# Kernel optimization log

Hardware: AMD Instinct MI355X
Metric: run time of the kernel (lower is better)

The kernel has to match this reference:

```python
import jax, jax.numpy as jnp
import numpy as np

B, T, C = 4, 2048, 1024
H, D = 16, 64  # num_heads, head_dim
WINDOW = 256


def setup_inputs() -> dict:
    key = jax.random.key(0)
    k_x, k_qkv, k_proj, k_qb, k_pb = jax.random.split(key, 5)
    x = jax.random.normal(k_x, (B, T, C), dtype=jnp.float32)
    # xavier-uniform-ish init for qkv weight (as in _reset_parameters)
    lim_qkv = float(np.sqrt(6.0 / (C + 3 * C)))
    qkv_w = jax.random.uniform(k_qkv, (3 * C, C), minval=-lim_qkv, maxval=lim_qkv, dtype=jnp.float32)
    qkv_b = jax.random.normal(k_qb, (3 * C,), dtype=jnp.float32) * 0.02
    lim_p = float(np.sqrt(1.0 / C))
    proj_w = jax.random.uniform(k_proj, (C, C), minval=-lim_p, maxval=lim_p, dtype=jnp.float32)
    proj_b = jax.random.normal(k_pb, (C,), dtype=jnp.float32) * 0.02
    # windowed causal mask: attend to j iff j <= i and i - j < WINDOW
    i = jnp.arange(T)[:, None]
    j = jnp.arange(T)[None, :]
    attn_mask = (j <= i) & (i - j < WINDOW)  # [T, T] bool
    return {"x": x, "attn_mask": attn_mask, "qkv_w": qkv_w, "qkv_b": qkv_b,
            "proj_w": proj_w, "proj_b": proj_b}


def reference(x, attn_mask, qkv_w, qkv_b, proj_w, proj_b):
    qkv = (x @ qkv_w.T + qkv_b).reshape(B, T, 3, H, D)
    qkv = jnp.transpose(qkv, (2, 0, 3, 1, 4))
    q, k, v = qkv[0], qkv[1], qkv[2]
    scale = 1.0 / jnp.sqrt(jnp.asarray(D, dtype=q.dtype))
    scores = jnp.einsum('bhqd,bhkd->bhqk', q, k) * scale  # [B,H,T,T]
    neg = jnp.asarray(jnp.finfo(scores.dtype).min, dtype=scores.dtype)
    scores = jnp.where(attn_mask[None, None], scores, neg)
    attn = jax.nn.softmax(scores, axis=-1)
    out = jnp.einsum('bhqk,bhkd->bhqd', attn, v)  # [B,H,T,D]
    out = jnp.transpose(out, (0, 2, 1, 3)).reshape(B, T, C)
    out = out @ proj_w.T + proj_b
    return out
```

## Files before the change

### kernel.cpp

```cpp
#include <hip/hip_runtime.h>

#define BB 4
#define TT 2048
#define CC 1024
#define HH 16
#define DD 64
#define WIN 256

typedef __attribute__((ext_vector_type(8))) short short8;
typedef __attribute__((ext_vector_type(4))) float floatx4;
typedef unsigned short u16;

typedef __attribute__((address_space(3))) void lds_void;
typedef const __attribute__((address_space(1))) void g_void;

__device__ __forceinline__ void gl_lds16(const u16* g, u16* l) {
    __builtin_amdgcn_global_load_lds((g_void*)g, (lds_void*)l, 16, 0, 0);
}

__device__ __forceinline__ float bf2f(u16 u) {
    union { unsigned int i; float f; } v; v.i = ((unsigned int)u) << 16; return v.f;
}
__device__ __forceinline__ u16 f2bf(float f) {
    union { float f; unsigned int i; } v; v.f = f;
    unsigned int x = v.i;
    x += ((x >> 16) & 1u) + 0x7FFFu;
    return (u16)(x >> 16);
}

__global__ void cvt_all(const float* __restrict__ x, const float* __restrict__ qw,
                        const float* __restrict__ pw,
                        u16* __restrict__ xb, u16* __restrict__ wb, u16* __restrict__ pwb) {
    int bid = blockIdx.x;
    const float* src; u16* dst; int off;
    if (bid < 4096)      { src = x;  dst = xb;  off = bid; }
    else if (bid < 5632) { src = qw; dst = wb;  off = bid - 4096; }
    else                 { src = pw; dst = pwb; off = bid - 5632; }
    int i = (off * 256 + (int)threadIdx.x) * 8;
    float4 a = *(const float4*)(src + i);
    float4 b = *(const float4*)(src + i + 4);
    u16 o[8] = { f2bf(a.x), f2bf(a.y), f2bf(a.z), f2bf(a.w),
                 f2bf(b.x), f2bf(b.y), f2bf(b.z), f2bf(b.w) };
    *(uint4*)(dst + i) = *(const uint4*)o;
}


__global__ __launch_bounds__(256) void gemm_qkv(
    const u16* __restrict__ A, const u16* __restrict__ Bw,
    const float* __restrict__ bias,
    u16* __restrict__ Qb, u16* __restrict__ Kb, u16* __restrict__ Vb)
{
    const int K = CC;
    __shared__ u16 As[4096];
    __shared__ u16 Bs[4096];
    const int tid = threadIdx.x;
    const int wave = tid >> 6, lane = tid & 63;
    const int wm = wave >> 1, wn = wave & 1;
    const int quad = lane >> 4, l15 = lane & 15;
    const int bN = blockIdx.x * 128, bM = blockIdx.y * 128;

    const int srow0 = wave * 16 + (lane >> 2);
    const int srow1 = (wave + 4) * 16 + (lane >> 2);
    const int schunk = ((lane & 3) ^ ((lane >> 3) & 3)) * 8;
    const u16* gA0 = A + (size_t)(bM + srow0) * K + schunk;
    const u16* gA1 = A + (size_t)(bM + srow1) * K + schunk;
    const u16* gB0 = Bw + (size_t)(bN + srow0) * K + schunk;
    const u16* gB1 = Bw + (size_t)(bN + srow1) * K + schunk;
    u16* lA0 = &As[wave * 512];
    u16* lA1 = &As[(wave + 4) * 512];
    u16* lB0 = &Bs[wave * 512];
    u16* lB1 = &Bs[(wave + 4) * 512];

    const int rdoff = l15 * 32 + ((quad ^ ((l15 >> 1) & 3)) * 8);

    floatx4 acc[4][4] = {};

    for (int k0 = 0; k0 < K; k0 += 32) {
        __syncthreads();
        gl_lds16(gA0 + k0, lA0);
        gl_lds16(gA1 + k0, lA1);
        gl_lds16(gB0 + k0, lB0);
        gl_lds16(gB1 + k0, lB1);
        __syncthreads();
        short8 af[4], bf[4];
#pragma unroll
        for (int i = 0; i < 4; ++i) {
            af[i] = *(const short8*)&As[(wm * 4 + i) * 512 + rdoff];
            bf[i] = *(const short8*)&Bs[(wn * 4 + i) * 512 + rdoff];
        }
#pragma unroll
        for (int mi = 0; mi < 4; ++mi)
#pragma unroll
            for (int ni = 0; ni < 4; ++ni)
                acc[mi][ni] = __builtin_amdgcn_mfma_f32_16x16x32_bf16(af[mi], bf[ni], acc[mi][ni], 0, 0, 0);
    }

#pragma unroll
    for (int mi = 0; mi < 4; ++mi)
#pragma unroll
        for (int ni = 0; ni < 4; ++ni) {
            int col = bN + wn * 64 + ni * 16 + l15;
            float bv = bias[col];
            int which = col >> 10, rem = col & 1023;
            int h = rem >> 6, d = rem & 63;
            u16* dst = which == 0 ? Qb : (which == 1 ? Kb : Vb);
#pragma unroll
            for (int rg = 0; rg < 4; ++rg) {
                int row = bM + wm * 64 + mi * 16 + quad * 4 + rg;
                int b = row >> 11, t = row & 2047;
                float v = acc[mi][ni][rg] + bv;
                dst[(((size_t)(b * HH + h)) * TT + t) * DD + d] = f2bf(v);
            }
        }
}

__global__ __launch_bounds__(256) void gemm_proj(
    const u16* __restrict__ A, const u16* __restrict__ Bw,
    const float* __restrict__ bias, float* __restrict__ Out)
{
    const int K = CC;
    __shared__ u16 As[4096];
    __shared__ u16 Bs[4096];
    const int tid = threadIdx.x;
    const int wave = tid >> 6, lane = tid & 63;
    const int wm = wave >> 1, wn = wave & 1;
    const int quad = lane >> 4, l15 = lane & 15;
    const int bN = blockIdx.x * 128, bM = blockIdx.y * 128;

    const int srow0 = wave * 16 + (lane >> 2);
    const int srow1 = (wave + 4) * 16 + (lane >> 2);
    const int schunk = ((lane & 3) ^ ((lane >> 3) & 3)) * 8;
    const u16* gA0 = A + (size_t)(bM + srow0) * K + schunk;
    const u16* gA1 = A + (size_t)(bM + srow1) * K + schunk;
    const u16* gB0 = Bw + (size_t)(bN + srow0) * K + schunk;
    const u16* gB1 = Bw + (size_t)(bN + srow1) * K + schunk;
    u16* lA0 = &As[wave * 512];
    u16* lA1 = &As[(wave + 4) * 512];
    u16* lB0 = &Bs[wave * 512];
    u16* lB1 = &Bs[(wave + 4) * 512];

    const int rdoff = l15 * 32 + ((quad ^ ((l15 >> 1) & 3)) * 8);

    floatx4 acc[4][4] = {};

    for (int k0 = 0; k0 < K; k0 += 32) {
        __syncthreads();
        gl_lds16(gA0 + k0, lA0);
        gl_lds16(gA1 + k0, lA1);
        gl_lds16(gB0 + k0, lB0);
        gl_lds16(gB1 + k0, lB1);
        __syncthreads();
        short8 af[4], bf[4];
#pragma unroll
        for (int i = 0; i < 4; ++i) {
            af[i] = *(const short8*)&As[(wm * 4 + i) * 512 + rdoff];
            bf[i] = *(const short8*)&Bs[(wn * 4 + i) * 512 + rdoff];
        }
#pragma unroll
        for (int mi = 0; mi < 4; ++mi)
#pragma unroll
            for (int ni = 0; ni < 4; ++ni)
                acc[mi][ni] = __builtin_amdgcn_mfma_f32_16x16x32_bf16(af[mi], bf[ni], acc[mi][ni], 0, 0, 0);
    }

#pragma unroll
    for (int mi = 0; mi < 4; ++mi)
#pragma unroll
        for (int ni = 0; ni < 4; ++ni) {
            int col = bN + wn * 64 + ni * 16 + l15;
            float bv = bias[col];
#pragma unroll
            for (int rg = 0; rg < 4; ++rg) {
                int row = bM + wm * 64 + mi * 16 + quad * 4 + rg;
                Out[(size_t)row * CC + col] = acc[mi][ni][rg] + bv;
            }
        }
}

__global__ __launch_bounds__(256) void attn_mfma(
    const u16* __restrict__ Qb, const u16* __restrict__ Kb, const u16* __restrict__ Vb,
    u16* __restrict__ Y)
{
    __shared__ u16 Ks[64][72];
    __shared__ u16 Vt[64][72];
    __shared__ u16 Ps[4][16][72];

    const int tid = threadIdx.x;
    const int wave = tid >> 6, lane = tid & 63;
    const int quad = lane >> 4, l15 = lane & 15;
    const int q0 = blockIdx.x * 64;
    const int bh = blockIdx.y;
    const int b = bh >> 4, h = bh & 15;
    const u16* Qp = Qb + (size_t)bh * TT * DD;
    const u16* Kp = Kb + (size_t)bh * TT * DD;
    const u16* Vp = Vb + (size_t)bh * TT * DD;
    const int qw = q0 + wave * 16;

    short8 qf[2];
    qf[0] = *(const short8*)&Qp[(size_t)(qw + l15) * DD + quad * 8];
    qf[1] = *(const short8*)&Qp[(size_t)(qw + l15) * DD + 32 + quad * 8];

    float m_i[4] = { -1e30f, -1e30f, -1e30f, -1e30f };
    float l_i[4] = { 0.f, 0.f, 0.f, 0.f };
    floatx4 Oacc[4] = {};

    const int kb = (q0 >= WIN) ? (q0 - WIN) : 0;
    for (int j0 = kb; j0 < q0 + 64; j0 += 64) {
        __syncthreads();
#pragma unroll
        for (int it = 0; it < 2; ++it) {
            int slot = tid + it * 256;
            int j = slot >> 3, c8 = (slot & 7) << 3;
            *(uint4*)&Ks[j][c8] = *(const uint4*)&Kp[(size_t)(j0 + j) * DD + c8];
        }
#pragma unroll
        for (int it = 0; it < 2; ++it) {
            int slot = tid + it * 256;
            int j = slot >> 3, d0 = (slot & 7) << 3;
            uint4 raw = *(const uint4*)&Vp[(size_t)(j0 + j) * DD + d0];
            const u16* u = (const u16*)&raw;
#pragma unroll
            for (int i = 0; i < 8; ++i) {
                int d = d0 + i;
                int col = (((j >> 3) ^ (d >> 3)) << 3) + (j & 7);
                Vt[d][col] = u[i];
            }
        }
        __syncthreads();

        floatx4 Sacc[4] = {};
#pragma unroll
        for (int nt = 0; nt < 4; ++nt) {
            short8 kf0 = *(const short8*)&Ks[nt * 16 + l15][quad * 8];
            short8 kf1 = *(const short8*)&Ks[nt * 16 + l15][32 + quad * 8];
            Sacc[nt] = __builtin_amdgcn_mfma_f32_16x16x32_bf16(qf[0], kf0, Sacc[nt], 0, 0, 0);
            Sacc[nt] = __builtin_amdgcn_mfma_f32_16x16x32_bf16(qf[1], kf1, Sacc[nt], 0, 0, 0);
        }

        float mc[4] = { -1e30f, -1e30f, -1e30f, -1e30f };
#pragma unroll
        for (int nt = 0; nt < 4; ++nt)
#pragma unroll
            for (int r = 0; r < 4; ++r) {
                int q = qw + quad * 4 + r;
                int j = j0 + nt * 16 + l15;
                float s = (j <= q && (q - j) < WIN) ? Sacc[nt][r] * 0.125f : -1e30f;
                Sacc[nt][r] = s;
                mc[r] = fmaxf(mc[r], s);
            }
#pragma unroll
        for (int m = 1; m < 16; m <<= 1)
#pragma unroll
            for (int r = 0; r < 4; ++r) mc[r] = fmaxf(mc[r], __shfl_xor(mc[r], m, 64));

        float alpha[4];
#pragma unroll
        for (int r = 0; r < 4; ++r) {
            float mn = fmaxf(m_i[r], mc[r]);
            alpha[r] = __expf(m_i[r] - mn);
            m_i[r] = mn;
        }
        float rs[4] = { 0.f, 0.f, 0.f, 0.f };
#pragma unroll
        for (int nt = 0; nt < 4; ++nt)
#pragma unroll
            for (int r = 0; r < 4; ++r) {
                float s = Sacc[nt][r];
                float p = (s > -1e29f) ? __expf(s - m_i[r]) : 0.f;
                Sacc[nt][r] = p;
                rs[r] += p;
            }
#pragma unroll
        for (int m = 1; m < 16; m <<= 1)
#pragma unroll
            for (int r = 0; r < 4; ++r) rs[r] += __shfl_xor(rs[r], m, 64);
#pragma unroll
        for (int r = 0; r < 4; ++r) l_i[r] = l_i[r] * alpha[r] + rs[r];
#pragma unroll
        for (int dt = 0; dt < 4; ++dt)
#pragma unroll
            for (int r = 0; r < 4; ++r) Oacc[dt][r] *= alpha[r];

#pragma unroll
        for (int nt = 0; nt < 4; ++nt)
#pragma unroll
            for (int r = 0; r < 4; ++r)
                Ps[wave][quad * 4 + r][nt * 16 + l15] = f2bf(Sacc[nt][r]);

#pragma unroll
        for (int ks = 0; ks < 2; ++ks) {
            short8 pf = *(const short8*)&Ps[wave][l15][ks * 32 + quad * 8];
#pragma unroll
            for (int dt = 0; dt < 4; ++dt) {
                int d = dt * 16 + l15;
                int col = (((ks * 4 + quad) ^ (d >> 3)) << 3);
                short8 vf = *(const short8*)&Vt[d][col];
                Oacc[dt] = __builtin_amdgcn_mfma_f32_16x16x32_bf16(pf, vf, Oacc[dt], 0, 0, 0);
            }
        }
    }

    float inv[4];
#pragma unroll
    for (int r = 0; r < 4; ++r) inv[r] = 1.f / l_i[r];
#pragma unroll
    for (int dt = 0; dt < 4; ++dt)
#pragma unroll
        for (int r = 0; r < 4; ++r) {
            int t = qw + quad * 4 + r;
            int d = dt * 16 + l15;
            Y[((size_t)b * TT + t) * CC + h * DD + d] = f2bf(Oacc[dt][r] * inv[r]);
        }
}

extern "C" void kernel_launch(void* const* d_in, const int* in_sizes, int n_in,
                              void* d_out, int out_size, void* d_ws, size_t ws_size,
                              hipStream_t stream) {
    const float* x      = (const float*)d_in[0];
    const float* qkv_w  = (const float*)d_in[2];
    const float* qkv_b  = (const float*)d_in[3];
    const float* proj_w = (const float*)d_in[4];
    const float* proj_b = (const float*)d_in[5];
    float* out = (float*)d_out;

    u16* xb  = (u16*)d_ws;
    u16* wb  = xb  + (size_t)8192 * 1024;
    u16* pwb = wb  + (size_t)3072 * 1024;
    u16* Qb  = pwb + (size_t)1024 * 1024;
    u16* Kb  = Qb  + (size_t)64 * 2048 * 64;
    u16* Vb  = Kb  + (size_t)64 * 2048 * 64;
    u16* Yb  = Vb  + (size_t)64 * 2048 * 64;

    cvt_all<<<6144, 256, 0, stream>>>(x, qkv_w, proj_w, xb, wb, pwb);
    gemm_qkv<<<dim3(24, 64), 256, 0, stream>>>(xb, wb, qkv_b, Qb, Kb, Vb);
    attn_mfma<<<dim3(TT / 64, BB * HH), 256, 0, stream>>>(Qb, Kb, Vb, Yb);
    gemm_proj<<<dim3(8, 64), 256, 0, stream>>>(Yb, pwb, proj_b, out);
}
```

Before: 238.3 us.

## Store V transposed from QKV GEMM and load K/V via direct global-to-LDS

The QKV GEMM epilogue now writes V in a [bh][d][t] transposed layout with packed 4-element stores, so the attention kernel no longer transposes V element by element through LDS. Attention loads K and V tiles with global_load_lds into swizzled LDS buffers and swaps the MFMA operand order so each lane owns one query row. That turns the row max and sum reductions into two shuffles on a single scalar and allows packed P and output stores. The V stores in the GEMM become strided across t, which may cost some write efficiency there.

```diff
diff --git a/kernel.cpp b/kernel.cpp
--- a/kernel.cpp
+++ b/kernel.cpp
@@ -44,11 +44,10 @@
     *(uint4*)(dst + i) = *(const uint4*)o;
 }
 
-
 __global__ __launch_bounds__(256) void gemm_qkv(
     const u16* __restrict__ A, const u16* __restrict__ Bw,
     const float* __restrict__ bias,
-    u16* __restrict__ Qb, u16* __restrict__ Kb, u16* __restrict__ Vb)
+    u16* __restrict__ Qb, u16* __restrict__ Kb, u16* __restrict__ Vtg)
 {
     const int K = CC;
     __shared__ u16 As[4096];
@@ -103,13 +102,18 @@
             float bv = bias[col];
             int which = col >> 10, rem = col & 1023;
             int h = rem >> 6, d = rem & 63;
-            u16* dst = which == 0 ? Qb : (which == 1 ? Kb : Vb);
-#pragma unroll
-            for (int rg = 0; rg < 4; ++rg) {
-                int row = bM + wm * 64 + mi * 16 + quad * 4 + rg;
-                int b = row >> 11, t = row & 2047;
-                float v = acc[mi][ni][rg] + bv;
-                dst[(((size_t)(b * HH + h)) * TT + t) * DD + d] = f2bf(v);
+            int row0 = bM + wm * 64 + mi * 16 + quad * 4;
+            int b = row0 >> 11, t0 = row0 & 2047;
+            if (which == 2) {
+                u16 pk[4];
+#pragma unroll
+                for (int rg = 0; rg < 4; ++rg) pk[rg] = f2bf(acc[mi][ni][rg] + bv);
+                *(uint2*)&Vtg[(((size_t)(b * HH + h)) * DD + d) * TT + t0] = *(const uint2*)pk;
+            } else {
+                u16* dst = which == 0 ? Qb : Kb;
+#pragma unroll
+                for (int rg = 0; rg < 4; ++rg)
+                    dst[(((size_t)(b * HH + h)) * TT + t0 + rg) * DD + d] = f2bf(acc[mi][ni][rg] + bv);
             }
         }
 }
@@ -178,12 +182,12 @@
 }
 
 __global__ __launch_bounds__(256) void attn_mfma(
-    const u16* __restrict__ Qb, const u16* __restrict__ Kb, const u16* __restrict__ Vb,
+    const u16* __restrict__ Qb, const u16* __restrict__ Kb, const u16* __restrict__ Vtg,
     u16* __restrict__ Y)
 {
-    __shared__ u16 Ks[64][72];
-    __shared__ u16 Vt[64][72];
-    __shared__ u16 Ps[4][16][72];
+    __shared__ __align__(16) u16 Ks[4096];
+    __shared__ __align__(16) u16 Vs[4096];
+    __shared__ __align__(16) u16 Ps[4][16][72];
 
     const int tid = threadIdx.x;
     const int wave = tid >> 6, lane = tid & 63;
@@ -193,124 +197,98 @@
     const int b = bh >> 4, h = bh & 15;
     const u16* Qp = Qb + (size_t)bh * TT * DD;
     const u16* Kp = Kb + (size_t)bh * TT * DD;
-    const u16* Vp = Vb + (size_t)bh * TT * DD;
+    const u16* Vp = Vtg + (size_t)bh * DD * TT;
     const int qw = q0 + wave * 16;
+
+    const int lrow = lane >> 3;
+    const int lchunk = ((lane & 7) ^ lrow) << 3;
+    const int s0 = wave * 2, s1 = wave * 2 + 1;
 
     short8 qf[2];
     qf[0] = *(const short8*)&Qp[(size_t)(qw + l15) * DD + quad * 8];
     qf[1] = *(const short8*)&Qp[(size_t)(qw + l15) * DD + 32 + quad * 8];
 
-    float m_i[4] = { -1e30f, -1e30f, -1e30f, -1e30f };
-    float l_i[4] = { 0.f, 0.f, 0.f, 0.f };
+    float m_i = -1e30f, l_i = 0.f;
     floatx4 Oacc[4] = {};
 
+    const int swz = l15 & 7;
     const int kb = (q0 >= WIN) ? (q0 - WIN) : 0;
     for (int j0 = kb; j0 < q0 + 64; j0 += 64) {
         __syncthreads();
-#pragma unroll
-        for (int it = 0; it < 2; ++it) {
-            int slot = tid + it * 256;
-            int j = slot >> 3, c8 = (slot & 7) << 3;
-            *(uint4*)&Ks[j][c8] = *(const uint4*)&Kp[(size_t)(j0 + j) * DD + c8];
-        }
-#pragma unroll
-        for (int it = 0; it < 2; ++it) {
-            int slot = tid + it * 256;
-            int j = slot >> 3, d0 = (slot & 7) << 3;
-            uint4 raw = *(const uint4*)&Vp[(size_t)(j0 + j) * DD + d0];
-            const u16* u = (const u16*)&raw;
-#pragma unroll
-            for (int i = 0; i < 8; ++i) {
-                int d = d0 + i;
-                int col = (((j >> 3) ^ (d >> 3)) << 3) + (j & 7);
-                Vt[d][col] = u[i];
-            }
-        }
+        gl_lds16(&Kp[(size_t)(j0 + s0 * 8 + lrow) * DD + lchunk], &Ks[s0 * 512]);
+        gl_lds16(&Kp[(size_t)(j0 + s1 * 8 + lrow) * DD + lchunk], &Ks[s1 * 512]);
+        gl_lds16(&Vp[(size_t)(s0 * 8 + lrow) * TT + j0 + lchunk], &Vs[s0 * 512]);
+        gl_lds16(&Vp[(size_t)(s1 * 8 + lrow) * TT + j0 + lchunk], &Vs[s1 * 512]);
         __syncthreads();
 
         floatx4 Sacc[4] = {};
 #pragma unroll
-        for (int nt = 0; nt < 4; ++nt) {
-            short8 kf0 = *(const short8*)&Ks[nt * 16 + l15][quad * 8];
-            short8 kf1 = *(const short8*)&Ks[nt * 16 + l15][32 + quad * 8];
-            Sacc[nt] = __builtin_amdgcn_mfma_f32_16x16x32_bf16(qf[0], kf0, Sacc[nt], 0, 0, 0);
-            Sacc[nt] = __builtin_amdgcn_mfma_f32_16x16x32_bf16(qf[1], kf1, Sacc[nt], 0, 0, 0);
-        }
-
-        float mc[4] = { -1e30f, -1e30f, -1e30f, -1e30f };
-#pragma unroll
-        for (int nt = 0; nt < 4; ++nt)
+        for (int ks = 0; ks < 2; ++ks)
+#pragma unroll
+            for (int kt = 0; kt < 4; ++kt) {
+                short8 kf = *(const short8*)&Ks[(kt * 16 + l15) * 64 + (((ks * 4 + quad) ^ swz) << 3)];
+                Sacc[kt] = __builtin_amdgcn_mfma_f32_16x16x32_bf16(kf, qf[ks], Sacc[kt], 0, 0, 0);
+            }
+
+        const int q = qw + l15;
+        float mc = -1e30f;
+#pragma unroll
+        for (int kt = 0; kt < 4; ++kt)
 #pragma unroll
             for (int r = 0; r < 4; ++r) {
-                int q = qw + quad * 4 + r;
-                int j = j0 + nt * 16 + l15;
-                float s = (j <= q && (q - j) < WIN) ? Sacc[nt][r] * 0.125f : -1e30f;
-                Sacc[nt][r] = s;
-                mc[r] = fmaxf(mc[r], s);
-            }
-#pragma unroll
-        for (int m = 1; m < 16; m <<= 1)
-#pragma unroll
-            for (int r = 0; r < 4; ++r) mc[r] = fmaxf(mc[r], __shfl_xor(mc[r], m, 64));
-
-        float alpha[4];
-#pragma unroll
-        for (int r = 0; r < 4; ++r) {
-            float mn = fmaxf(m_i[r], mc[r]);
-            alpha[r] = __expf(m_i[r] - mn);
-            m_i[r] = mn;
-        }
-        float rs[4] = { 0.f, 0.f, 0.f, 0.f };
-#pragma unroll
-        for (int nt = 0; nt < 4; ++nt)
+                int j = j0 + kt * 16 + quad * 4 + r;
+                float s = (j <= q && (q - j) < WIN) ? Sacc[kt][r] * 0.125f : -1e30f;
+                Sacc[kt][r] = s;
+                mc = fmaxf(mc, s);
+            }
+        mc = fmaxf(mc, __shfl_xor(mc, 16, 64));
+        mc = fmaxf(mc, __shfl_xor(mc, 32, 64));
+
+        float mn = fmaxf(m_i, mc);
+        float alpha = __expf(m_i - mn);
+        m_i = mn;
+
+        float rs = 0.f;
+#pragma unroll
+        for (int kt = 0; kt < 4; ++kt) {
+            u16 pk[4];
 #pragma unroll
             for (int r = 0; r < 4; ++r) {
-                float s = Sacc[nt][r];
-                float p = (s > -1e29f) ? __expf(s - m_i[r]) : 0.f;
-                Sacc[nt][r] = p;
-                rs[r] += p;
-            }
-#pragma unroll
-        for (int m = 1; m < 16; m <<= 1)
-#pragma unroll
-            for (int r = 0; r < 4; ++r) rs[r] += __shfl_xor(rs[r], m, 64);
-#pragma unroll
-        for (int r = 0; r < 4; ++r) l_i[r] = l_i[r] * alpha[r] + rs[r];
+                float s = Sacc[kt][r];
+                float p = (s > -1e29f) ? __expf(s - m_i) : 0.f;
+                rs += p;
+                pk[r] = f2bf(p);
+            }
+            *(uint2*)&Ps[wave][l15][kt * 16 + quad * 4] = *(const uint2*)pk;
+        }
+        rs += __shfl_xor(rs, 16, 64);
+        rs += __shfl_xor(rs, 32, 64);
+        l_i = l_i * alpha + rs;
 #pragma unroll
         for (int dt = 0; dt < 4; ++dt)
 #pragma unroll
-            for (int r = 0; r < 4; ++r) Oacc[dt][r] *= alpha[r];
-
-#pragma unroll
-        for (int nt = 0; nt < 4; ++nt)
-#pragma unroll
-            for (int r = 0; r < 4; ++r)
-                Ps[wave][quad * 4 + r][nt * 16 + l15] = f2bf(Sacc[nt][r]);
+            for (int r = 0; r < 4; ++r) Oacc[dt][r] *= alpha;
 
 #pragma unroll
         for (int ks = 0; ks < 2; ++ks) {
             short8 pf = *(const short8*)&Ps[wave][l15][ks * 32 + quad * 8];
 #pragma unroll
             for (int dt = 0; dt < 4; ++dt) {
-                int d = dt * 16 + l15;
-                int col = (((ks * 4 + quad) ^ (d >> 3)) << 3);
-                short8 vf = *(const short8*)&Vt[d][col];
-                Oacc[dt] = __builtin_amdgcn_mfma_f32_16x16x32_bf16(pf, vf, Oacc[dt], 0, 0, 0);
+                short8 vf = *(const short8*)&Vs[(dt * 16 + l15) * 64 + (((ks * 4 + quad) ^ swz) << 3)];
+                Oacc[dt] = __builtin_amdgcn_mfma_f32_16x16x32_bf16(vf, pf, Oacc[dt], 0, 0, 0);
             }
         }
     }
 
-    float inv[4];
-#pragma unroll
-    for (int r = 0; r < 4; ++r) inv[r] = 1.f / l_i[r];
-#pragma unroll
-    for (int dt = 0; dt < 4; ++dt)
-#pragma unroll
-        for (int r = 0; r < 4; ++r) {
-            int t = qw + quad * 4 + r;
-            int d = dt * 16 + l15;
-            Y[((size_t)b * TT + t) * CC + h * DD + d] = f2bf(Oacc[dt][r] * inv[r]);
-        }
+    float inv = 1.f / l_i;
+    const int t = qw + l15;
+#pragma unroll
+    for (int dt = 0; dt < 4; ++dt) {
+        u16 o[4];
+#pragma unroll
+        for (int r = 0; r < 4; ++r) o[r] = f2bf(Oacc[dt][r] * inv);
+        *(uint2*)&Y[((size_t)b * TT + t) * CC + h * DD + dt * 16 + quad * 4] = *(const uint2*)o;
+    }
 }
 
 extern "C" void kernel_launch(void* const* d_in, const int* in_sizes, int n_in,
@@ -328,11 +306,11 @@
     u16* pwb = wb  + (size_t)3072 * 1024;
     u16* Qb  = pwb + (size_t)1024 * 1024;
     u16* Kb  = Qb  + (size_t)64 * 2048 * 64;
-    u16* Vb  = Kb  + (size_t)64 * 2048 * 64;
-    u16* Yb  = Vb  + (size_t)64 * 2048 * 64;
+    u16* Vtg = Kb  + (size_t)64 * 2048 * 64;
+    u16* Yb  = Vtg + (size_t)64 * 2048 * 64;
 
     cvt_all<<<6144, 256, 0, stream>>>(x, qkv_w, proj_w, xb, wb, pwb);
-    gemm_qkv<<<dim3(24, 64), 256, 0, stream>>>(xb, wb, qkv_b, Qb, Kb, Vb);
-    attn_mfma<<<dim3(TT / 64, BB * HH), 256, 0, stream>>>(Qb, Kb, Vb, Yb);
+    gemm_qkv<<<dim3(24, 64), 256, 0, stream>>>(xb, wb, qkv_b, Qb, Kb, Vtg);
+    attn_mfma<<<dim3(TT / 64, BB * HH), 256, 0, stream>>>(Qb, Kb, Vtg, Yb);
     gemm_proj<<<dim3(8, 64), 256, 0, stream>>>(Yb, pwb, proj_b, out);
 }
```

Measured after the change: 244.2 us. +2.5%, slower.
